# Kernel tuning notes

Measured on AMD Instinct MI355X. Metric: run time of the kernel, lower is better.

## Reference

```python
import jax, jax.numpy as jnp
import numpy as np

B, T, H, D = 256, 256, 16, 88  # batch, max_length, hidden_dim, data_dim (88 piano tones)


def setup_inputs() -> dict:
    key = jax.random.key(0)
    k1, k2, k3, k4 = jax.random.split(key, 4)
    sequences = jax.random.randint(k1, (B, T, D), 0, 2).astype(jnp.float32)  # binary tones
    lengths = jax.random.randint(k2, (B,), T // 2, T + 1).astype(jnp.int32)
    # probs_x: sticky transition matrix on the simplex (pyro init: 0.9*I + 0.1*ones, normalized)
    px = 0.9 * jnp.eye(H) + 0.1 * jnp.ones((H, H)) + 0.01 * jax.random.uniform(k3, (H, H))
    probs_x = px / px.sum(-1, keepdims=True)
    # probs_y: Bernoulli emission probs in the open unit interval, indexed [x_t, y_{t-1,d}, d]
    probs_y = jax.random.uniform(k4, (H, 2, D), minval=0.05, maxval=0.95)
    return {"sequences": sequences, "lengths": lengths,
            "probs_x": probs_x, "probs_y": probs_y}


def reference(sequences, lengths, probs_x, probs_y):
    # HMM forward algorithm == pyro parallel enumeration of x_t with masked Bernoulli obs.
    Bn, Tn, Dn = sequences.shape
    Hn = probs_x.shape[0]
    scale = 1.0
    mask = jnp.arange(Tn)[None, :] < lengths[:, None]                      # (B,T)
    # previous observation (y_{-1} = 0), observed so it is data, not a latent
    yprev = jnp.concatenate([jnp.zeros((Bn, 1, Dn), sequences.dtype),
                             sequences[:, :-1]], axis=1)                   # (B,T,D)
    # p[b,t,h,d] = probs_y[h, yprev[b,t,d], d]  (binary gather via where)
    p = jnp.where(yprev[:, :, None, :] > 0.5,
                  probs_y[None, None, :, 1, :],
                  probs_y[None, None, :, 0, :])                            # (B,T,H,D)
    y = sequences[:, :, None, :]
    emit = jnp.sum(y * jnp.log(p) + (1.0 - y) * jnp.log1p(-p), axis=-1)    # (B,T,H)
    emit = jnp.where(mask[:, :, None], emit, 0.0)                          # masked obs -> logprob 0
    log_trans = jnp.log(probs_x)                                           # (H,H)
    # x starts at state 0
    alpha0 = jnp.broadcast_to(jnp.where(jnp.arange(Hn) == 0, 0.0, -1e9), (Bn, Hn))

    def step(alpha, inp):
        emit_t, mask_t = inp                                               # (B,H), (B,)
        a_on = jax.nn.logsumexp(alpha[:, :, None] + log_trans[None], axis=1) + emit_t
        # masked step: transition factor = 1 for all states -> uniform carry
        a_off = jnp.broadcast_to(jax.nn.logsumexp(alpha, axis=-1, keepdims=True), alpha.shape)
        return jnp.where(mask_t[:, None], a_on, a_off), None

    alpha, _ = jax.lax.scan(step, alpha0, (emit.transpose(1, 0, 2), mask.T))
    return scale * jnp.sum(jax.nn.logsumexp(alpha, axis=-1))
```

## Files before the change

kernel.cpp:

```cpp
#include <hip/hip_runtime.h>

#define Bn 256
#define Tn 256
#define Hn 16
#define Dn 88
#define LOG16 2.7725887222397811f
#define SB 104

typedef _Float16 v4h __attribute__((ext_vector_type(4)));
typedef _Float16 v8h __attribute__((ext_vector_type(8)));
typedef float    v4f __attribute__((ext_vector_type(4)));

template<int CTRL>
__device__ __forceinline__ float dppf(float x) {
    return __int_as_float(__builtin_amdgcn_update_dpp(
        0, __float_as_int(x), CTRL, 0xF, 0xF, true));
}
__device__ __forceinline__ float rowsum16(float v) {
    v += dppf<0x128>(v); v += dppf<0x124>(v);
    v += dppf<0x122>(v); v += dppf<0x121>(v);
    return v;
}
__device__ __forceinline__ float rowmax16(float v) {
    v = fmaxf(v, dppf<0x128>(v)); v = fmaxf(v, dppf<0x124>(v));
    v = fmaxf(v, dppf<0x122>(v)); v = fmaxf(v, dppf<0x121>(v));
    return v;
}

#if __has_builtin(__builtin_amdgcn_mfma_f32_16x16x16f16)
#define KSTEPS 6
#define KW 16
typedef v4h fragT;
#define MFMA(a,b,c) __builtin_amdgcn_mfma_f32_16x16x16f16(a, b, c, 0, 0, 0)
#else
#define KSTEPS 3
#define KW 32
typedef v8h fragT;
#define MFMA(a,b,c) __builtin_amdgcn_mfma_f32_16x16x32_f16(a, b, c, 0, 0, 0)
#endif

__global__ __launch_bounds__(256) void emit_kernel(
    const float* __restrict__ seq,
    const int*   __restrict__ lengths,
    const float* __restrict__ probs_y,
    float* __restrict__ EG,
    float* __restrict__ MsumG,
    float* __restrict__ out)
{
    __shared__ __align__(16) float4 ldsbuf[9554];
    unsigned char* lds = (unsigned char*)ldsbuf;
    unsigned short*     Cb   = (unsigned short*)lds;
    _Float16*           CbH  = (_Float16*)lds;
    unsigned long long* C64  = (unsigned long long*)lds;
    _Float16*           Am   = (_Float16*)(lds + 53456);
    float*              basep   = (float*)(lds + 62672);
    float*              msumAcc = (float*)(lds + 62736);
    float4*             raw  = (float4*)(lds + 62752);
    _Float16*           CPH  = (_Float16*)(lds + 62752);
    uint4*              Cv4  = (uint4*)lds;
    uint4*              CPv4 = (uint4*)(lds + 62752);

    const int tid = threadIdx.x;
    const int b = blockIdx.x;
    if (tid == 0) *msumAcc = 0.0f;
    if (b == 0 && tid == 1) out[0] = 0.0f;
    const float4* seqv = (const float4*)(seq + (size_t)b * Tn * Dn);

#if __has_builtin(__builtin_amdgcn_global_load_lds)
    {
        const int w = tid >> 6, l = tid & 63;
        #pragma unroll
        for (int k = 0; k < 22; ++k) {
            const int f = (w * 22 + k) * 64 + l;
            __builtin_amdgcn_global_load_lds(
                (const __attribute__((address_space(1))) unsigned int*)(seqv + f),
                (__attribute__((address_space(3))) unsigned int*)(raw + f),
                16, 0, 0);
        }
    }
#else
    #pragma unroll
    for (int k = 0; k < 22; ++k) raw[tid + (k << 8)] = seqv[tid + (k << 8)];
#endif

    {
        const int n = tid >> 4, ks = tid & 15;
        float bsum = 0.0f;
        #pragma unroll
        for (int jj = 0; jj < 6; ++jj) {
            int k = ks + 16 * jj;
            float a1 = 0.f, a2 = 0.f, a3 = 0.f;
            if (k < Dn) {
                float p0 = probs_y[(n * 2 + 0) * Dn + k];
                float p1 = probs_y[(n * 2 + 1) * Dn + k];
                float l00 = __logf(1.0f - p0), l01 = __logf(p0);
                float l10 = __logf(1.0f - p1), l11 = __logf(p1);
                a1 = l01 - l00; a2 = l10 - l00; a3 = l11 - l10 - l01 + l00;
                bsum += l00;
            }
            Am[0 * 1536 + n * 96 + k] = (_Float16)a1;
            Am[1 * 1536 + n * 96 + k] = (_Float16)a2;
            Am[2 * 1536 + n * 96 + k] = (_Float16)a3;
        }
        bsum = rowsum16(bsum);
        if (ks == 0) basep[n] = bsum;
    }
    if (tid < 26) C64[tid] = 0ull;
    {
        const int r = tid + 1;
        C64[r * 26 + 22] = 0ull; C64[r * 26 + 23] = 0ull;
        C64[r * 26 + 24] = 0ull; C64[r * 26 + 25] = 0ull;
    }
    __syncthreads();

    #pragma unroll
    for (int k = 0; k < 22; ++k) {
        const int f = tid + (k << 8);
        float4 v = raw[f];
        int t = f / 22, jj = f - t * 22;
        unsigned lo = (v.x > 0.5f ? 0x3C00u : 0u) | (v.y > 0.5f ? 0x3C000000u : 0u);
        unsigned hi = (v.z > 0.5f ? 0x3C00u : 0u) | (v.w > 0.5f ? 0x3C000000u : 0u);
        C64[(t + 1) * 26 + jj] = (unsigned long long)lo |
                                 ((unsigned long long)hi << 32);
    }
    __syncthreads();

    {
        const int r = tid + 1;
        #pragma unroll
        for (int k = 0; k < 13; ++k) {
            uint4 a = Cv4[r * 13 + k];
            uint4 p = Cv4[(r - 1) * 13 + k];
            uint4 o;
            o.x = a.x & p.x; o.y = a.y & p.y; o.z = a.z & p.z; o.w = a.w & p.w;
            CPv4[r * 13 + k] = o;
        }
    }
    __syncthreads();

    const int len = min(max(lengths[b], 0), Tn);
    const int w = tid >> 6, m = tid & 15, q = (tid >> 4) & 3;
    float* EGf = EG + ((size_t)(b >> 4)) * 65536 + (size_t)(b & 15) * 16;

    fragT B1f[KSTEPS], B2f[KSTEPS], B3f[KSTEPS];
    #pragma unroll
    for (int ks = 0; ks < KSTEPS; ++ks) {
        const int off = m * 96 + ks * KW + (KW / 4) * q;
        B1f[ks] = *(const fragT*)(Am + 0 * 1536 + off);
        B2f[ks] = *(const fragT*)(Am + 1 * 1536 + off);
        B3f[ks] = *(const fragT*)(Am + 2 * 1536 + off);
    }
    const float bh = basep[m];
    float ms = 0.0f;

    #pragma unroll
    for (int j = 0; j < 4; ++j) {
        const int tile = (w * 4 + j) * 16;
        v4f aC = {0.f, 0.f, 0.f, 0.f}, aP = aC, aCP = aC;
        #pragma unroll
        for (int ks = 0; ks < KSTEPS; ++ks) {
            const int co = ks * KW + (KW / 4) * q;
            fragT fC  = *(const fragT*)(CbH + (tile + m + 1) * SB + co);
            fragT fP  = *(const fragT*)(CbH + (tile + m) * SB + co);
            fragT fCP = *(const fragT*)(CPH + (tile + m + 1) * SB + co);
            aC  = MFMA(fC,  B1f[ks], aC);
            aP  = MFMA(fP,  B2f[ks], aP);
            aCP = MFMA(fCP, B3f[ks], aCP);
        }
        #pragma unroll
        for (int i = 0; i < 4; ++i) {
            const int t = tile + 4 * q + i;
            float em = aC[i] + aP[i] + aCP[i] + bh;
            float mx = rowmax16(em);
            float E = (t < len) ? __expf(em - mx) : 1.0f;
            EGf[(size_t)t * 256 + m] = E;
            if (m == 0) ms += (t < len) ? mx : 0.0f;
        }
    }
    if (m == 0) atomicAdd(msumAcc, ms);
    __syncthreads();
    if (tid == 0) MsumG[b] = *msumAcc;
}

__global__ __launch_bounds__(64) void forward_kernel(
    const float* __restrict__ EG,
    const float* __restrict__ MsumG,
    const float* __restrict__ probs_x,
    const int*   __restrict__ lengths,
    float* __restrict__ out)
{
    const int lane = threadIdx.x & 63;
    const int q = lane >> 4, n = lane & 15;
    const int g = blockIdx.x;
    const int b = g * 16 + n;

#if __has_builtin(__builtin_amdgcn_mfma_f32_16x16x16f16)
    v4h A;
    #pragma unroll
    for (int i = 0; i < 4; ++i) A[i] = (_Float16)probs_x[(4 * q + i) * Hn + n];
    v4h Bv;
    #pragma unroll
    for (int i = 0; i < 4; ++i) Bv[i] = (_Float16)0.0f;
    if (q == 0) Bv[0] = (_Float16)1.0f;
#else
    v8h A;
    #pragma unroll
    for (int j = 0; j < 8; ++j) {
        int k = 8 * q + j;
        A[j] = (k < Hn) ? (_Float16)probs_x[k * Hn + n] : (_Float16)0.0f;
    }
    v8h Bv;
    #pragma unroll
    for (int j = 0; j < 8; ++j) Bv[j] = (_Float16)0.0f;
    if (q == 0) Bv[0] = (_Float16)1.0f;
#endif

    float L = MsumG[b];
    const float4* Ep = (const float4*)EG + (g * Tn * 16 + n) * 4 + q;

    float4 ebuf[8];
    #pragma unroll
    for (int k = 0; k < 8; ++k) ebuf[k] = Ep[k * 64];

    float4 dm = {0.f, 0.f, 0.f, 0.f};
    #pragma unroll 8
    for (int t = 0; t < Tn; ++t) {
        float4 e = ebuf[t & 7];
        int tn = t + 8; tn = (tn < Tn) ? tn : (Tn - 1);
        ebuf[t & 7] = Ep[tn * 64];

        v4f z = {0.f, 0.f, 0.f, 0.f};
#if __has_builtin(__builtin_amdgcn_mfma_f32_16x16x16f16)
        v4f D = __builtin_amdgcn_mfma_f32_16x16x16f16(A, Bv, z, 0, 0, 0);
#else
        v4f D = __builtin_amdgcn_mfma_f32_16x16x32_f16(A, Bv, z, 0, 0, 0);
#endif
        dm.x = D[0] * e.x; dm.y = D[1] * e.y;
        dm.z = D[2] * e.z; dm.w = D[3] * e.w;

        if ((t & 3) == 3) {
            float s = dm.x + dm.y + dm.z + dm.w;
            s += __shfl_xor(s, 16);
            s += __shfl_xor(s, 32);
            float rr = 1.0f / s;
            dm.x *= rr; dm.y *= rr; dm.z *= rr; dm.w *= rr;
            L += __logf(s);
        }

#if __has_builtin(__builtin_amdgcn_mfma_f32_16x16x16f16)
        Bv[0] = (_Float16)dm.x; Bv[1] = (_Float16)dm.y;
        Bv[2] = (_Float16)dm.z; Bv[3] = (_Float16)dm.w;
#else
        v4h hv;
        hv[0] = (_Float16)dm.x; hv[1] = (_Float16)dm.y;
        hv[2] = (_Float16)dm.z; hv[3] = (_Float16)dm.w;
        unsigned u0 = ((unsigned*)&hv)[0], u1 = ((unsigned*)&hv)[1];
        int src0 = ((2 * q) << 4) + n, src1 = ((2 * q + 1) << 4) + n;
        unsigned a0 = __shfl((int)u0, src0), a1 = __shfl((int)u1, src0);
        unsigned b0 = __shfl((int)u0, src1), b1 = __shfl((int)u1, src1);
        unsigned uu[4];
        uu[0] = (q < 2) ? a0 : 0u; uu[1] = (q < 2) ? a1 : 0u;
        uu[2] = (q < 2) ? b0 : 0u; uu[3] = (q < 2) ? b1 : 0u;
        Bv = *(v8h*)uu;
#endif
    }

    float S = dm.x + dm.y + dm.z + dm.w;
    S += __shfl_xor(S, 16);
    S += __shfl_xor(S, 32);
    int len = min(max(lengths[b], 0), Tn);
    float res = L + __logf(S) + (float)(Tn - len) * LOG16;
    res = rowsum16(q == 0 ? res : 0.0f);
    if (lane == 0) atomicAdd(out, res);
}

extern "C" void kernel_launch(void* const* d_in, const int* in_sizes, int n_in,
                              void* d_out, int out_size, void* d_ws, size_t ws_size,
                              hipStream_t stream) {
    const float* seq     = (const float*)d_in[0];
    const int*   lengths = (const int*)  d_in[1];
    const float* probs_x = (const float*)d_in[2];
    const float* probs_y = (const float*)d_in[3];
    float* out   = (float*)d_out;
    float* EG    = (float*)d_ws;
    float* MsumG = EG + (size_t)Bn * Tn * Hn;

    emit_kernel<<<Bn, 256, 0, stream>>>(seq, lengths, probs_y, EG, MsumG, out);
    forward_kernel<<<Bn / 16, 64, 0, stream>>>(EG, MsumG, probs_x, lengths, out);
}
```

Before: 101.2 us.

## Fuse emission and forward passes, split time scan into parallel segment matrix products

Merges the emission kernel and the forward recursion into one kernel per batch element, keeping emissions in LDS instead of a global workspace. Each of the four waves computes a 16x16 transfer matrix for its 64-step segment by running the recursion with an identity start. A final pass composes the four segment matrices with DPP gathers. This removes the global round trip, the second launch, and the 256-step serial chain over 16 blocks. The cost is four times the MFMA work per step, an extra memset launch, and greater fp16 rounding risk from propagating full matrices.

```diff
diff --git a/kernel.cpp b/kernel.cpp
--- a/kernel.cpp
+++ b/kernel.cpp
@@ -16,6 +16,16 @@
     return __int_as_float(__builtin_amdgcn_update_dpp(
         0, __float_as_int(x), CTRL, 0xF, 0xF, true));
 }
+#define GATHER16(dst, s)                                                     \
+    dst[0] = (s);                                                            \
+    dst[1] = dppf<0x128>(dst[0]);                                            \
+    dst[2] = dppf<0x124>(dst[0]); dst[3]  = dppf<0x124>(dst[1]);             \
+    dst[4] = dppf<0x122>(dst[0]); dst[5]  = dppf<0x122>(dst[1]);             \
+    dst[6] = dppf<0x122>(dst[2]); dst[7]  = dppf<0x122>(dst[3]);             \
+    dst[8] = dppf<0x121>(dst[0]); dst[9]  = dppf<0x121>(dst[1]);             \
+    dst[10] = dppf<0x121>(dst[2]); dst[11] = dppf<0x121>(dst[3]);            \
+    dst[12] = dppf<0x121>(dst[4]); dst[13] = dppf<0x121>(dst[5]);            \
+    dst[14] = dppf<0x121>(dst[6]); dst[15] = dppf<0x121>(dst[7]);
 __device__ __forceinline__ float rowsum16(float v) {
     v += dppf<0x128>(v); v += dppf<0x124>(v);
     v += dppf<0x122>(v); v += dppf<0x121>(v);
@@ -39,44 +49,43 @@
 #define MFMA(a,b,c) __builtin_amdgcn_mfma_f32_16x16x32_f16(a, b, c, 0, 0, 0)
 #endif
 
-__global__ __launch_bounds__(256) void emit_kernel(
+__global__ __launch_bounds__(256) void fused_kernel(
     const float* __restrict__ seq,
     const int*   __restrict__ lengths,
+    const float* __restrict__ probs_x,
     const float* __restrict__ probs_y,
-    float* __restrict__ EG,
-    float* __restrict__ MsumG,
     float* __restrict__ out)
 {
-    __shared__ __align__(16) float4 ldsbuf[9554];
+    __shared__ __align__(16) float4 ldsbuf[9555];
     unsigned char* lds = (unsigned char*)ldsbuf;
-    unsigned short*     Cb   = (unsigned short*)lds;
     _Float16*           CbH  = (_Float16*)lds;
     unsigned long long* C64  = (unsigned long long*)lds;
+    uint4*              Cv4  = (uint4*)lds;
     _Float16*           Am   = (_Float16*)(lds + 53456);
     float*              basep   = (float*)(lds + 62672);
     float*              msumAcc = (float*)(lds + 62736);
-    float4*             raw  = (float4*)(lds + 62752);
-    _Float16*           CPH  = (_Float16*)(lds + 62752);
-    uint4*              Cv4  = (uint4*)lds;
-    uint4*              CPv4 = (uint4*)(lds + 62752);
+    float*              Lseg    = (float*)(lds + 62740);
+    float4*             raw  = (float4*)(lds + 62768);
+    _Float16*           CPH  = (_Float16*)(lds + 62768);
+    uint4*              CPv4 = (uint4*)(lds + 62768);
+    float*              Esh  = (float*)(lds + 116224);
+    float*              Msh  = (float*)(lds + 132608);
 
     const int tid = threadIdx.x;
     const int b = blockIdx.x;
+    const int w = tid >> 6, lane = tid & 63;
+    const int q = lane >> 4, m = lane & 15;
     if (tid == 0) *msumAcc = 0.0f;
-    if (b == 0 && tid == 1) out[0] = 0.0f;
     const float4* seqv = (const float4*)(seq + (size_t)b * Tn * Dn);
 
 #if __has_builtin(__builtin_amdgcn_global_load_lds)
-    {
-        const int w = tid >> 6, l = tid & 63;
-        #pragma unroll
-        for (int k = 0; k < 22; ++k) {
-            const int f = (w * 22 + k) * 64 + l;
-            __builtin_amdgcn_global_load_lds(
-                (const __attribute__((address_space(1))) unsigned int*)(seqv + f),
-                (__attribute__((address_space(3))) unsigned int*)(raw + f),
-                16, 0, 0);
-        }
+    #pragma unroll
+    for (int k = 0; k < 22; ++k) {
+        const int f = (w * 22 + k) * 64 + lane;
+        __builtin_amdgcn_global_load_lds(
+            (const __attribute__((address_space(1))) unsigned int*)(seqv + f),
+            (__attribute__((address_space(3))) unsigned int*)(raw + f),
+            16, 0, 0);
     }
 #else
     #pragma unroll
@@ -139,139 +148,143 @@
     __syncthreads();
 
     const int len = min(max(lengths[b], 0), Tn);
-    const int w = tid >> 6, m = tid & 15, q = (tid >> 4) & 3;
-    float* EGf = EG + ((size_t)(b >> 4)) * 65536 + (size_t)(b & 15) * 16;
-
-    fragT B1f[KSTEPS], B2f[KSTEPS], B3f[KSTEPS];
-    #pragma unroll
-    for (int ks = 0; ks < KSTEPS; ++ks) {
-        const int off = m * 96 + ks * KW + (KW / 4) * q;
-        B1f[ks] = *(const fragT*)(Am + 0 * 1536 + off);
-        B2f[ks] = *(const fragT*)(Am + 1 * 1536 + off);
-        B3f[ks] = *(const fragT*)(Am + 2 * 1536 + off);
-    }
-    const float bh = basep[m];
-    float ms = 0.0f;
-
-    #pragma unroll
-    for (int j = 0; j < 4; ++j) {
-        const int tile = (w * 4 + j) * 16;
-        v4f aC = {0.f, 0.f, 0.f, 0.f}, aP = aC, aCP = aC;
+    {
+        fragT B1f[KSTEPS], B2f[KSTEPS], B3f[KSTEPS];
         #pragma unroll
         for (int ks = 0; ks < KSTEPS; ++ks) {
-            const int co = ks * KW + (KW / 4) * q;
-            fragT fC  = *(const fragT*)(CbH + (tile + m + 1) * SB + co);
-            fragT fP  = *(const fragT*)(CbH + (tile + m) * SB + co);
-            fragT fCP = *(const fragT*)(CPH + (tile + m + 1) * SB + co);
-            aC  = MFMA(fC,  B1f[ks], aC);
-            aP  = MFMA(fP,  B2f[ks], aP);
-            aCP = MFMA(fCP, B3f[ks], aCP);
-        }
-        #pragma unroll
-        for (int i = 0; i < 4; ++i) {
-            const int t = tile + 4 * q + i;
-            float em = aC[i] + aP[i] + aCP[i] + bh;
-            float mx = rowmax16(em);
-            float E = (t < len) ? __expf(em - mx) : 1.0f;
-            EGf[(size_t)t * 256 + m] = E;
-            if (m == 0) ms += (t < len) ? mx : 0.0f;
-        }
-    }
-    if (m == 0) atomicAdd(msumAcc, ms);
-    __syncthreads();
-    if (tid == 0) MsumG[b] = *msumAcc;
-}
-
-__global__ __launch_bounds__(64) void forward_kernel(
-    const float* __restrict__ EG,
-    const float* __restrict__ MsumG,
-    const float* __restrict__ probs_x,
-    const int*   __restrict__ lengths,
-    float* __restrict__ out)
-{
-    const int lane = threadIdx.x & 63;
-    const int q = lane >> 4, n = lane & 15;
-    const int g = blockIdx.x;
-    const int b = g * 16 + n;
-
+            const int off = m * 96 + ks * KW + (KW / 4) * q;
+            B1f[ks] = *(const fragT*)(Am + 0 * 1536 + off);
+            B2f[ks] = *(const fragT*)(Am + 1 * 1536 + off);
+            B3f[ks] = *(const fragT*)(Am + 2 * 1536 + off);
+        }
+        const float bh = basep[m];
+        float ms = 0.0f;
+        #pragma unroll
+        for (int j = 0; j < 4; ++j) {
+            const int tile = (w * 4 + j) * 16;
+            v4f aC = {0.f, 0.f, 0.f, 0.f}, aP = aC, aCP = aC;
+            #pragma unroll
+            for (int ks = 0; ks < KSTEPS; ++ks) {
+                const int co = ks * KW + (KW / 4) * q;
+                fragT fC  = *(const fragT*)(CbH + (tile + m + 1) * SB + co);
+                fragT fP  = *(const fragT*)(CbH + (tile + m) * SB + co);
+                fragT fCP = *(const fragT*)(CPH + (tile + m + 1) * SB + co);
+                aC  = MFMA(fC,  B1f[ks], aC);
+                aP  = MFMA(fP,  B2f[ks], aP);
+                aCP = MFMA(fCP, B3f[ks], aCP);
+            }
+            #pragma unroll
+            for (int i = 0; i < 4; ++i) {
+                const int t = tile + 4 * q + i;
+                float em = aC[i] + aP[i] + aCP[i] + bh;
+                float mx = rowmax16(em);
+                float E = (t < len) ? __expf(em - mx) : 1.0f;
+                Esh[t * 16 + m] = E;
+                if (m == 0) ms += (t < len) ? mx : 0.0f;
+            }
+        }
+        if (m == 0) atomicAdd(msumAcc, ms);
+    }
+    __syncthreads();
+
+    {
 #if __has_builtin(__builtin_amdgcn_mfma_f32_16x16x16f16)
-    v4h A;
-    #pragma unroll
-    for (int i = 0; i < 4; ++i) A[i] = (_Float16)probs_x[(4 * q + i) * Hn + n];
-    v4h Bv;
-    #pragma unroll
-    for (int i = 0; i < 4; ++i) Bv[i] = (_Float16)0.0f;
-    if (q == 0) Bv[0] = (_Float16)1.0f;
+        v4h A2;
+        #pragma unroll
+        for (int i = 0; i < 4; ++i) A2[i] = (_Float16)probs_x[(4 * q + i) * Hn + m];
+        v4h Sv;
+        #pragma unroll
+        for (int i = 0; i < 4; ++i) Sv[i] = (_Float16)((4 * q + i == m) ? 1.0f : 0.0f);
 #else
-    v8h A;
-    #pragma unroll
-    for (int j = 0; j < 8; ++j) {
-        int k = 8 * q + j;
-        A[j] = (k < Hn) ? (_Float16)probs_x[k * Hn + n] : (_Float16)0.0f;
-    }
-    v8h Bv;
-    #pragma unroll
-    for (int j = 0; j < 8; ++j) Bv[j] = (_Float16)0.0f;
-    if (q == 0) Bv[0] = (_Float16)1.0f;
+        v8h A2;
+        #pragma unroll
+        for (int jj = 0; jj < 8; ++jj) {
+            int k = 8 * q + jj;
+            A2[jj] = (k < Hn) ? (_Float16)probs_x[k * Hn + m] : (_Float16)0.0f;
+        }
+        v8h Sv;
+        #pragma unroll
+        for (int jj = 0; jj < 8; ++jj) {
+            int k = 8 * q + jj;
+            Sv[jj] = (_Float16)((k < Hn && k == m) ? 1.0f : 0.0f);
+        }
 #endif
-
-    float L = MsumG[b];
-    const float4* Ep = (const float4*)EG + (g * Tn * 16 + n) * 4 + q;
-
-    float4 ebuf[8];
-    #pragma unroll
-    for (int k = 0; k < 8; ++k) ebuf[k] = Ep[k * 64];
-
-    float4 dm = {0.f, 0.f, 0.f, 0.f};
-    #pragma unroll 8
-    for (int t = 0; t < Tn; ++t) {
-        float4 e = ebuf[t & 7];
-        int tn = t + 8; tn = (tn < Tn) ? tn : (Tn - 1);
-        ebuf[t & 7] = Ep[tn * 64];
-
-        v4f z = {0.f, 0.f, 0.f, 0.f};
+        float Lw = 0.0f;
+        const int t0 = w << 6;
+        const float4* EshV = (const float4*)Esh;
+        float4 eb[8];
+        #pragma unroll
+        for (int k = 0; k < 8; ++k) eb[k] = EshV[(t0 + k) * 4 + q];
+
+        float4 dm = {0.f, 0.f, 0.f, 0.f};
+        #pragma unroll 8
+        for (int tl = 0; tl < 64; ++tl) {
+            float4 e = eb[tl & 7];
+            int tn = tl + 8; tn = (tn < 64) ? tn : 63;
+            eb[tl & 7] = EshV[(t0 + tn) * 4 + q];
+
+            v4f z = {0.f, 0.f, 0.f, 0.f};
+            v4f D = MFMA(A2, Sv, z);
+            dm.x = D[0] * e.x; dm.y = D[1] * e.y;
+            dm.z = D[2] * e.z; dm.w = D[3] * e.w;
+
+            if ((tl & 3) == 3) {
+                float s = dm.x + dm.y + dm.z + dm.w;
+                s += __shfl_xor(s, 1);  s += __shfl_xor(s, 2);
+                s += __shfl_xor(s, 4);  s += __shfl_xor(s, 8);
+                s += __shfl_xor(s, 16); s += __shfl_xor(s, 32);
+                float rr = 1.0f / s;
+                dm.x *= rr; dm.y *= rr; dm.z *= rr; dm.w *= rr;
+                Lw += __logf(s);
+            }
 #if __has_builtin(__builtin_amdgcn_mfma_f32_16x16x16f16)
-        v4f D = __builtin_amdgcn_mfma_f32_16x16x16f16(A, Bv, z, 0, 0, 0);
+            Sv[0] = (_Float16)dm.x; Sv[1] = (_Float16)dm.y;
+            Sv[2] = (_Float16)dm.z; Sv[3] = (_Float16)dm.w;
 #else
-        v4f D = __builtin_amdgcn_mfma_f32_16x16x32_f16(A, Bv, z, 0, 0, 0);
+            v4h hv;
+            hv[0] = (_Float16)dm.x; hv[1] = (_Float16)dm.y;
+            hv[2] = (_Float16)dm.z; hv[3] = (_Float16)dm.w;
+            unsigned u0 = ((unsigned*)&hv)[0], u1 = ((unsigned*)&hv)[1];
+            int src0 = ((2 * q) << 4) + m, src1 = ((2 * q + 1) << 4) + m;
+            unsigned a0 = __shfl((int)u0, src0), a1 = __shfl((int)u1, src0);
+            unsigned b0 = __shfl((int)u0, src1), b1 = __shfl((int)u1, src1);
+            unsigned uu[4];
+            uu[0] = (q < 2) ? a0 : 0u; uu[1] = (q < 2) ? a1 : 0u;
+            uu[2] = (q < 2) ? b0 : 0u; uu[3] = (q < 2) ? b1 : 0u;
+            Sv = *(v8h*)uu;
 #endif
-        dm.x = D[0] * e.x; dm.y = D[1] * e.y;
-        dm.z = D[2] * e.z; dm.w = D[3] * e.w;
-
-        if ((t & 3) == 3) {
-            float s = dm.x + dm.y + dm.z + dm.w;
-            s += __shfl_xor(s, 16);
-            s += __shfl_xor(s, 32);
-            float rr = 1.0f / s;
-            dm.x *= rr; dm.y *= rr; dm.z *= rr; dm.w *= rr;
-            L += __logf(s);
-        }
-
-#if __has_builtin(__builtin_amdgcn_mfma_f32_16x16x16f16)
-        Bv[0] = (_Float16)dm.x; Bv[1] = (_Float16)dm.y;
-        Bv[2] = (_Float16)dm.z; Bv[3] = (_Float16)dm.w;
-#else
-        v4h hv;
-        hv[0] = (_Float16)dm.x; hv[1] = (_Float16)dm.y;
-        hv[2] = (_Float16)dm.z; hv[3] = (_Float16)dm.w;
-        unsigned u0 = ((unsigned*)&hv)[0], u1 = ((unsigned*)&hv)[1];
-        int src0 = ((2 * q) << 4) + n, src1 = ((2 * q + 1) << 4) + n;
-        unsigned a0 = __shfl((int)u0, src0), a1 = __shfl((int)u1, src0);
-        unsigned b0 = __shfl((int)u0, src1), b1 = __shfl((int)u1, src1);
-        unsigned uu[4];
-        uu[0] = (q < 2) ? a0 : 0u; uu[1] = (q < 2) ? a1 : 0u;
-        uu[2] = (q < 2) ? b0 : 0u; uu[3] = (q < 2) ? b1 : 0u;
-        Bv = *(v8h*)uu;
-#endif
-    }
-
-    float S = dm.x + dm.y + dm.z + dm.w;
-    S += __shfl_xor(S, 16);
-    S += __shfl_xor(S, 32);
-    int len = min(max(lengths[b], 0), Tn);
-    float res = L + __logf(S) + (float)(Tn - len) * LOG16;
-    res = rowsum16(q == 0 ? res : 0.0f);
-    if (lane == 0) atomicAdd(out, res);
+        }
+        Msh[w * 256 + (4 * q + 0) * 16 + m] = dm.x;
+        Msh[w * 256 + (4 * q + 1) * 16 + m] = dm.y;
+        Msh[w * 256 + (4 * q + 2) * 16 + m] = dm.z;
+        Msh[w * 256 + (4 * q + 3) * 16 + m] = dm.w;
+        if (lane == 0) Lseg[w] = Lw;
+    }
+    __syncthreads();
+
+    if (tid >= 64) return;
+    const int j = tid & 15;
+    float cal[16];
+    GATHER16(cal, (float)j);
+    int ci[16];
+    #pragma unroll
+    for (int k = 0; k < 16; ++k) ci[k] = (int)cal[k];
+
+    float alpha = (j == 0) ? 1.0f : 0.0f;
+    #pragma unroll
+    for (int s = 0; s < 4; ++s) {
+        float y[16];
+        GATHER16(y, alpha);
+        const float* Mr = Msh + s * 256 + j * 16;
+        float acc = y[0] * Mr[ci[0]];
+        #pragma unroll
+        for (int k = 1; k < 16; ++k) acc = fmaf(y[k], Mr[ci[k]], acc);
+        alpha = acc;
+    }
+    float S = rowsum16(alpha);
+    float res = *msumAcc + Lseg[0] + Lseg[1] + Lseg[2] + Lseg[3]
+              + __logf(S) + (float)(Tn - len) * LOG16;
+    if (tid == 0) atomicAdd(out, res);
 }
 
 extern "C" void kernel_launch(void* const* d_in, const int* in_sizes, int n_in,
@@ -281,10 +294,8 @@
     const int*   lengths = (const int*)  d_in[1];
     const float* probs_x = (const float*)d_in[2];
     const float* probs_y = (const float*)d_in[3];
-    float* out   = (float*)d_out;
-    float* EG    = (float*)d_ws;
-    float* MsumG = EG + (size_t)Bn * Tn * Hn;
-
-    emit_kernel<<<Bn, 256, 0, stream>>>(seq, lengths, probs_y, EG, MsumG, out);
-    forward_kernel<<<Bn / 16, 64, 0, stream>>>(EG, MsumG, probs_x, lengths, out);
-}
+    float* out = (float*)d_out;
+
+    hipMemsetAsync(d_out, 0, sizeof(float) * out_size, stream);
+    fused_kernel<<<Bn, 256, 0, stream>>>(seq, lengths, probs_x, probs_y, out);
+}
```

New measurement: 88.47 us. 12.6% less time.
